# Optimization experiments

Measured on AMD Instinct MI355X. Metric: run time of the kernel, lower is better.

Reference implementation:

```python
import jax, jax.numpy as jnp
import numpy as np

V, E, H, L, B, T = 32000, 256, 512, 2, 64, 2048


def setup_inputs() -> dict:
    key = jax.random.key(0)
    ks = jax.random.split(key, 24)
    def rn(i, shape, scale=0.05):
        return jax.random.normal(ks[i], shape, jnp.float32) * scale
    inp = {
        "token": jax.random.randint(ks[0], (B,), 0, V),
        "h0": rn(1, (L, B, H), 1.0),
        "c0": rn(2, (L, B, H), 1.0),
        "encoder_outputs": rn(3, (B, T, H), 1.0),
        "mask": jax.random.randint(ks[4], (B, T), 0, 2).astype(jnp.int32),
        # parameters
        "emb_table": rn(5, (V, E), 1.0).at[0].set(0.0),  # padding_idx=0
        "W_attn": rn(6, (H, 2 * H)),
        "b_attn": rn(7, (H,)),
        "v_attn": jax.random.uniform(ks[8], (H,), jnp.float32),  # torch.rand init
        "W_ih0": rn(9, (4 * H, E + H)),
        "W_hh0": rn(10, (4 * H, H)),
        "b_ih0": rn(11, (4 * H,)),
        "b_hh0": rn(12, (4 * H,)),
        "W_ih1": rn(13, (4 * H, H)),
        "W_hh1": rn(14, (4 * H, H)),
        "b_ih1": rn(15, (4 * H,)),
        "b_hh1": rn(16, (4 * H,)),
        "W_out": rn(17, (V, H)),
        "b_out": rn(18, (V,)),
    }
    return inp


def _lstm_step(x, h, c, Wi, Wh, bi, bh):
    # PyTorch gate order: i, f, g, o
    gates = x @ Wi.T + bi + h @ Wh.T + bh  # [B, 4H]
    i, f, g, o = jnp.split(gates, 4, axis=-1)
    c_new = jax.nn.sigmoid(f) * c + jax.nn.sigmoid(i) * jnp.tanh(g)
    h_new = jax.nn.sigmoid(o) * jnp.tanh(c_new)
    return h_new, c_new


def reference(token, h0, c0, encoder_outputs, mask,
              emb_table, W_attn, b_attn, v_attn,
              W_ih0, W_hh0, b_ih0, b_hh0,
              W_ih1, W_hh1, b_ih1, b_hh1,
              W_out, b_out):
    embedded = emb_table[token]  # [B, E]

    # Bahdanau attention using the top-layer hidden state.
    # Linear on concat(hidden, enc) split into two matmuls (no T-tiling of hidden).
    h_top = h0[-1]  # [B, H]
    h_part = h_top @ W_attn[:, :H].T  # [B, H]
    e_part = jnp.einsum('bth,kh->btk', encoder_outputs, W_attn[:, H:])  # [B, T, H]
    energy = jnp.tanh(h_part[:, None, :] + e_part + b_attn) @ v_attn  # [B, T]
    energy = jnp.where(mask == 0, -jnp.inf, energy)
    attn_weights = jax.nn.softmax(energy, axis=1)  # [B, T]

    context = jnp.einsum('bt,bth->bh', attn_weights, encoder_outputs)  # [B, H]

    # Single-step 2-layer LSTM (eval mode: no inter-layer dropout).
    x0 = jnp.concatenate([embedded, context], axis=-1)  # [B, E+H]
    h0_new, c0_new = _lstm_step(x0, h0[0], c0[0], W_ih0, W_hh0, b_ih0, b_hh0)
    h1_new, c1_new = _lstm_step(h0_new, h0[1], c0[1], W_ih1, W_hh1, b_ih1, b_hh1)

    logits = h1_new @ W_out.T + b_out  # [B, V]
    h_new = jnp.stack([h0_new, h1_new])  # [L, B, H]
    c_new = jnp.stack([c0_new, c1_new])
    return logits, (h_new, c_new), attn_weights
```

## Files before the change

### kernel.cpp

```cpp
#include <hip/hip_runtime.h>
#include <hip/hip_fp16.h>
#include <cmath>

typedef _Float16 f16x8 __attribute__((ext_vector_type(8)));
typedef _Float16 f16x4 __attribute__((ext_vector_type(4)));
typedef float f32x4 __attribute__((ext_vector_type(4)));

#define NV 32000
#define NE 256
#define NH 512
#define NB 64
#define NT 2048

__device__ __forceinline__ float fast_tanh(float x) {
  return 1.f - 2.f / (__expf(2.f * x) + 1.f);
}
__device__ __forceinline__ float fast_sig(float x) {
  return 1.f / (1.f + __expf(-x));
}

__global__ void k_swz_be(const float* __restrict__ Wattn, _Float16* __restrict__ Be) {
  int idx = blockIdx.x * 256 + threadIdx.x;
  int l = idx & 63, nt = (idx >> 6) & 31, kc = idx >> 11;
  int n = (nt << 4) + (l & 15);
  int h0 = (kc << 5) + ((l >> 4) << 3);
  const float* s = Wattn + n * 1024 + 512 + h0;
  _Float16* d = Be + idx * 8;
  #pragma unroll
  for (int j = 0; j < 8; ++j) d[j] = (_Float16)s[j];
}

__global__ void k_prep_htop(const float* __restrict__ h0, _Float16* __restrict__ xh,
                            _Float16* __restrict__ xcat1) {
  int b = blockIdx.x, t = threadIdx.x;
  _Float16 v = (_Float16)h0[NB * NH + b * NH + t];
  xh[b * NH + t] = v;
  xcat1[b * 1024 + 512 + t] = v;
}

template <int KLEN>
__global__ __launch_bounds__(128)
void k_gemm_bT(const _Float16* __restrict__ A, int K,
               const float* __restrict__ B0, int ldb0,
               const float* __restrict__ B1, int ldb1, int b1k,
               const float* __restrict__ bias,
               float* __restrict__ out, int N) {
  int ntiles = N >> 5;
  int bn = blockIdx.x % ntiles, kcid = blockIdx.x / ntiles;
  int tid = threadIdx.x, w = tid >> 6, l = tid & 63;
  int n = (bn << 5) + (w << 4) + (l & 15);
  int kq = (l >> 4) << 3;
  int k0 = kcid * KLEN;
  f32x4 acc[4];
  #pragma unroll
  for (int mi = 0; mi < 4; ++mi) acc[mi] = (f32x4){0.f, 0.f, 0.f, 0.f};
  #pragma unroll 2
  for (int kk = 0; kk < KLEN; kk += 32) {
    int kbase = k0 + kk;
    f16x8 a[4];
    #pragma unroll
    for (int mi = 0; mi < 4; ++mi)
      a[mi] = *(const f16x8*)(A + (size_t)((l & 15) + (mi << 4)) * K + kbase + kq);
    const float* bp;
    if (B1 && kbase >= b1k) bp = B1 + (size_t)n * ldb1 + (kbase - b1k) + kq;
    else                    bp = B0 + (size_t)n * ldb0 + kbase + kq;
    float4 x0 = *(const float4*)bp;
    float4 x1 = *(const float4*)(bp + 4);
    f16x8 bf = {(_Float16)x0.x, (_Float16)x0.y, (_Float16)x0.z, (_Float16)x0.w,
                (_Float16)x1.x, (_Float16)x1.y, (_Float16)x1.z, (_Float16)x1.w};
    #pragma unroll
    for (int mi = 0; mi < 4; ++mi)
      acc[mi] = __builtin_amdgcn_mfma_f32_16x16x32_f16(a[mi], bf, acc[mi], 0, 0, 0);
  }
  float* op = out + (size_t)kcid * 64 * N;
  #pragma unroll
  for (int mi = 0; mi < 4; ++mi)
    #pragma unroll
    for (int r = 0; r < 4; ++r) {
      int row = (mi << 4) + ((l >> 4) << 2) + r;
      float v = acc[mi][r];
      if (bias) v += bias[n];
      op[(size_t)row * N + n] = v;
    }
}

__global__ __launch_bounds__(512, 4)
void k_energy(const float* __restrict__ enc, const _Float16* __restrict__ Be,
              const float* __restrict__ hp0, const float* __restrict__ hp1,
              const float* __restrict__ battn, const float* __restrict__ vat,
              const int* __restrict__ mask,
              float* __restrict__ eng, float* __restrict__ mcsc,
              float* __restrict__ numpart) {
  __shared__ _Float16 As[64 * 512];
  __shared__ float hpl[NH], vl[NH], ep[64][8], wl[64];
  int tile = blockIdx.x;
  int b = tile >> 5;
  long row0 = (long)tile << 6;
  int tid = threadIdx.x;
  hpl[tid] = hp0[(b << 9) + tid] + hp1[(b << 9) + tid] + battn[tid];
  vl[tid] = vat[tid];
  int w = tid >> 6, l = tid & 63;

  const float4* encp = (const float4*)(enc + row0 * NH);
  for (int half = 0; half < 2; ++half) {
    float4 st[8];
    #pragma unroll
    for (int i = 0; i < 8; ++i) st[i] = encp[tid + ((half * 8 + i) << 9)];
    #pragma unroll
    for (int i = 0; i < 8; ++i) {
      int s = tid + ((half * 8 + i) << 9);
      int r = s >> 7, c4 = s & 127;
      f16x4 h4 = {(_Float16)st[i].x, (_Float16)st[i].y,
                  (_Float16)st[i].z, (_Float16)st[i].w};
      *(f16x4*)((char*)As + (r << 10) + (((c4 << 3)) ^ ((r & 7) << 4))) = h4;
    }
  }
  __syncthreads();

  f32x4 acc[4][4];
  #pragma unroll
  for (int mi = 0; mi < 4; ++mi)
    #pragma unroll
    for (int ni = 0; ni < 4; ++ni) acc[mi][ni] = (f32x4){0.f, 0.f, 0.f, 0.f};

  for (int kc = 0; kc < 16; ++kc) {
    f16x8 a[4], bf[4];
    int kb = (kc << 6) + ((l >> 4) << 4);
    #pragma unroll
    for (int mi = 0; mi < 4; ++mi) {
      int r = (mi << 4) + (l & 15);
      a[mi] = *(const f16x8*)((char*)As + (r << 10) + (kb ^ ((r & 7) << 4)));
    }
    #pragma unroll
    for (int ni = 0; ni < 4; ++ni)
      bf[ni] = *(const f16x8*)(Be + (size_t)((((kc << 5) + (w << 2) + ni) << 6) + l) * 8);
    #pragma unroll
    for (int mi = 0; mi < 4; ++mi)
      #pragma unroll
      for (int ni = 0; ni < 4; ++ni)
        acc[mi][ni] = __builtin_amdgcn_mfma_f32_16x16x32_f16(a[mi], bf[ni], acc[mi][ni], 0, 0, 0);
  }

  int cl = l & 15;
  #pragma unroll
  for (int mi = 0; mi < 4; ++mi) {
    float s0 = 0.f, s1 = 0.f, s2 = 0.f, s3 = 0.f;
    #pragma unroll
    for (int ni = 0; ni < 4; ++ni) {
      int col = (w << 6) + (ni << 4) + cl;
      float hv = hpl[col], vv = vl[col];
      s0 += vv * fast_tanh(acc[mi][ni][0] + hv);
      s1 += vv * fast_tanh(acc[mi][ni][1] + hv);
      s2 += vv * fast_tanh(acc[mi][ni][2] + hv);
      s3 += vv * fast_tanh(acc[mi][ni][3] + hv);
    }
    #pragma unroll
    for (int off = 1; off < 16; off <<= 1) {
      s0 += __shfl_xor(s0, off, 64);
      s1 += __shfl_xor(s1, off, 64);
      s2 += __shfl_xor(s2, off, 64);
      s3 += __shfl_xor(s3, off, 64);
    }
    if (cl == 0) {
      int rb = (mi << 4) + ((l >> 4) << 2);
      ep[rb][w] = s0; ep[rb + 1][w] = s1; ep[rb + 2][w] = s2; ep[rb + 3][w] = s3;
    }
  }
  __syncthreads();

  if (tid < 64) {
    float e = 0.f;
    #pragma unroll
    for (int q = 0; q < 8; ++q) e += ep[tid][q];
    int mk = mask[row0 + tid];
    e = mk ? e : -3.0e38f;
    eng[row0 + tid] = e;
    float m = e;
    #pragma unroll
    for (int off = 32; off; off >>= 1) m = fmaxf(m, __shfl_xor(m, off, 64));
    float wv = mk ? __expf(e - m) : 0.f;
    float s = wv;
    #pragma unroll
    for (int off = 32; off; off >>= 1) s += __shfl_xor(s, off, 64);
    wl[tid] = wv;
    if (tid == 0) { mcsc[tile * 2] = m; mcsc[tile * 2 + 1] = s; }
  }
  __syncthreads();

  float a = 0.f;
  #pragma unroll 4
  for (int t = 0; t < 64; ++t) {
    float ev = (float)(*(const _Float16*)((char*)As + (t << 10) + (((tid * 2)) ^ ((t & 7) << 4))));
    a += wl[t] * ev;
  }
  numpart[(size_t)tile * NH + tid] = a;
}

__global__ void k_combine(const float* __restrict__ mcsc, const float* __restrict__ numpart,
                          const float* __restrict__ eng, const int* __restrict__ token,
                          const float* __restrict__ emb, const float* __restrict__ h0,
                          _Float16* __restrict__ xcat0, float* __restrict__ attw) {
  __shared__ float scale_s[32], Ms, dens;
  int b = blockIdx.x, tid = threadIdx.x;
  if (tid < 32) {
    float m = mcsc[(b * 32 + tid) * 2];
    float s = mcsc[(b * 32 + tid) * 2 + 1];
    float M = m;
    #pragma unroll
    for (int off = 16; off; off >>= 1) M = fmaxf(M, __shfl_xor(M, off, 32));
    float sc = __expf(m - M);
    float d = sc * s;
    #pragma unroll
    for (int off = 16; off; off >>= 1) d += __shfl_xor(d, off, 32);
    scale_s[tid] = sc;
    if (tid == 0) { Ms = M; dens = d; }
  }
  __syncthreads();
  float M = Ms, rden = 1.f / dens;
  float a = 0.f;
  #pragma unroll 4
  for (int c = 0; c < 32; ++c) a += scale_s[c] * numpart[(size_t)(b * 32 + c) * NH + tid];
  xcat0[b * 1280 + 256 + tid] = (_Float16)(a * rden);
  if (tid < 256) xcat0[b * 1280 + tid] = (_Float16)emb[(size_t)token[b] * NE + tid];
  xcat0[b * 1280 + 768 + tid] = (_Float16)h0[b * NH + tid];
  #pragma unroll
  for (int i = 0; i < 4; ++i) {
    int t = tid + (i << 9);
    attw[(b << 11) + t] = __expf(eng[(b << 11) + t] - M) * rden;
  }
}

__global__ void k_act(const float* __restrict__ pg, const float* __restrict__ bih,
                      const float* __restrict__ bhh, const float* __restrict__ cprev,
                      float* __restrict__ hout, float* __restrict__ cout,
                      _Float16* __restrict__ hf16, int hpitch, int nchunks) {
  int idx = blockIdx.x * 256 + threadIdx.x;
  int b = idx >> 9, u = idx & 511;
  float g[4];
  #pragma unroll
  for (int gi = 0; gi < 4; ++gi) {
    float s = bih[gi * 512 + u] + bhh[gi * 512 + u];
    for (int kc = 0; kc < nchunks; ++kc)
      s += pg[((size_t)kc * 64 + b) * 2048 + gi * 512 + u];
    g[gi] = s;
  }
  float c = fast_sig(g[1]) * cprev[idx] + fast_sig(g[0]) * fast_tanh(g[2]);
  float h = fast_sig(g[3]) * fast_tanh(c);
  cout[idx] = c;
  hout[idx] = h;
  hf16[b * hpitch + u] = (_Float16)h;
}

extern "C" void kernel_launch(void* const* d_in, const int* in_sizes, int n_in,
                              void* d_out, int out_size, void* d_ws, size_t ws_size,
                              hipStream_t stream) {
  (void)in_sizes; (void)n_in; (void)out_size; (void)ws_size;
  const int*   token = (const int*)d_in[0];
  const float* h0    = (const float*)d_in[1];
  const float* c0    = (const float*)d_in[2];
  const float* enc   = (const float*)d_in[3];
  const int*   mask  = (const int*)d_in[4];
  const float* emb   = (const float*)d_in[5];
  const float* Wattn = (const float*)d_in[6];
  const float* battn = (const float*)d_in[7];
  const float* vattn = (const float*)d_in[8];
  const float* Wih0  = (const float*)d_in[9];
  const float* Whh0  = (const float*)d_in[10];
  const float* bih0  = (const float*)d_in[11];
  const float* bhh0  = (const float*)d_in[12];
  const float* Wih1  = (const float*)d_in[13];
  const float* Whh1  = (const float*)d_in[14];
  const float* bih1  = (const float*)d_in[15];
  const float* bhh1  = (const float*)d_in[16];
  const float* Wout  = (const float*)d_in[17];
  const float* bout  = (const float*)d_in[18];

  float* ws    = (float*)d_ws;
  float* pghp  = ws;
  float* eng   = pghp + 65536;
  float* mcsc  = eng + 131072;
  float* np    = mcsc + 4096;
  float* pg0   = np + 1048576;
  float* pg1   = pg0 + 524288;
  _Float16* Be    = (_Float16*)(pg1 + 524288);
  _Float16* xh    = Be + 262144;
  _Float16* xcat0 = xh + 32768;
  _Float16* xcat1 = xcat0 + 81920;
  _Float16* h1f   = xcat1 + 65536;

  float* out    = (float*)d_out;
  float* logits = out;
  float* hnew   = out + (size_t)NB * NV;
  float* cnew   = hnew + 2 * NB * NH;
  float* attw   = cnew + 2 * NB * NH;

  k_swz_be<<<dim3(128), dim3(256), 0, stream>>>(Wattn, Be);
  k_prep_htop<<<dim3(64), dim3(512), 0, stream>>>(h0, xh, xcat1);
  k_gemm_bT<256><<<dim3(32), dim3(128), 0, stream>>>(
      xh, NH, Wattn, 1024, nullptr, 0, 1 << 30, nullptr, pghp, NH);
  k_energy<<<dim3(2048), dim3(512), 0, stream>>>(
      enc, Be, pghp, pghp + 32768, battn, vattn, mask, eng, mcsc, np);
  k_combine<<<dim3(64), dim3(512), 0, stream>>>(
      mcsc, np, eng, token, emb, h0, xcat0, attw);
  k_gemm_bT<320><<<dim3(256), dim3(128), 0, stream>>>(
      xcat0, 1280, Wih0, 768, Whh0, NH, 768, nullptr, pg0, 2048);
  k_act<<<dim3(128), dim3(256), 0, stream>>>(
      pg0, bih0, bhh0, c0, hnew, cnew, xcat1, 1024, 4);
  k_gemm_bT<256><<<dim3(256), dim3(128), 0, stream>>>(
      xcat1, 1024, Wih1, NH, Whh1, NH, NH, nullptr, pg1, 2048);
  k_act<<<dim3(128), dim3(256), 0, stream>>>(
      pg1, bih1, bhh1, c0 + NB * NH, hnew + NB * NH, cnew + NB * NH, h1f, 512, 4);
  k_gemm_bT<512><<<dim3(1000), dim3(128), 0, stream>>>(
      h1f, NH, Wout, NH, nullptr, 0, 1 << 30, bout, logits, NV);
}
```

Baseline: 193.6 us.

## Stream encoder tile from global into MFMA fragments instead of LDS staging

The energy kernel no longer converts the whole 64x512 encoder tile to fp16 in shared memory. Each wave now loads its A fragments straight from global memory and converts them in registers, using a 2x4 wave grid with 2x8 MFMA tiles per wave. The context partial sum is recomputed in fp32 by re-reading the encoder rows from global memory, which is expected to hit cache, and is reduced through a small shared buffer. This frees about 64KB of LDS per block to raise occupancy and removes the staging barrier. The cost is strided global fragment loads and a second pass over the encoder tile.

```diff
diff --git a/kernel.cpp b/kernel.cpp
--- a/kernel.cpp
+++ b/kernel.cpp
@@ -91,63 +91,52 @@
               const int* __restrict__ mask,
               float* __restrict__ eng, float* __restrict__ mcsc,
               float* __restrict__ numpart) {
-  __shared__ _Float16 As[64 * 512];
-  __shared__ float hpl[NH], vl[NH], ep[64][8], wl[64];
+  __shared__ float hpl[NH], vl[NH], ep[64][4], wl[64], psc[4][NH];
   int tile = blockIdx.x;
   int b = tile >> 5;
   long row0 = (long)tile << 6;
-  int tid = threadIdx.x;
+  int tid = threadIdx.x, w = tid >> 6, l = tid & 63;
+  int wm = w >> 2, wn = w & 3;
   hpl[tid] = hp0[(b << 9) + tid] + hp1[(b << 9) + tid] + battn[tid];
   vl[tid] = vat[tid];
-  int w = tid >> 6, l = tid & 63;
-
-  const float4* encp = (const float4*)(enc + row0 * NH);
-  for (int half = 0; half < 2; ++half) {
-    float4 st[8];
-    #pragma unroll
-    for (int i = 0; i < 8; ++i) st[i] = encp[tid + ((half * 8 + i) << 9)];
-    #pragma unroll
-    for (int i = 0; i < 8; ++i) {
-      int s = tid + ((half * 8 + i) << 9);
-      int r = s >> 7, c4 = s & 127;
-      f16x4 h4 = {(_Float16)st[i].x, (_Float16)st[i].y,
-                  (_Float16)st[i].z, (_Float16)st[i].w};
-      *(f16x4*)((char*)As + (r << 10) + (((c4 << 3)) ^ ((r & 7) << 4))) = h4;
-    }
-  }
   __syncthreads();
 
-  f32x4 acc[4][4];
-  #pragma unroll
-  for (int mi = 0; mi < 4; ++mi)
-    #pragma unroll
-    for (int ni = 0; ni < 4; ++ni) acc[mi][ni] = (f32x4){0.f, 0.f, 0.f, 0.f};
-
+  const float* Ab = enc + (row0 + (wm << 5) + (l & 15)) * NH + ((l >> 4) << 3);
+  f32x4 acc[2][8];
+  #pragma unroll
+  for (int mi = 0; mi < 2; ++mi)
+    #pragma unroll
+    for (int ni = 0; ni < 8; ++ni) acc[mi][ni] = (f32x4){0.f, 0.f, 0.f, 0.f};
+
+  #pragma unroll 2
   for (int kc = 0; kc < 16; ++kc) {
-    f16x8 a[4], bf[4];
-    int kb = (kc << 6) + ((l >> 4) << 4);
-    #pragma unroll
-    for (int mi = 0; mi < 4; ++mi) {
-      int r = (mi << 4) + (l & 15);
-      a[mi] = *(const f16x8*)((char*)As + (r << 10) + (kb ^ ((r & 7) << 4)));
-    }
-    #pragma unroll
-    for (int ni = 0; ni < 4; ++ni)
-      bf[ni] = *(const f16x8*)(Be + (size_t)((((kc << 5) + (w << 2) + ni) << 6) + l) * 8);
-    #pragma unroll
-    for (int mi = 0; mi < 4; ++mi)
-      #pragma unroll
-      for (int ni = 0; ni < 4; ++ni)
-        acc[mi][ni] = __builtin_amdgcn_mfma_f32_16x16x32_f16(a[mi], bf[ni], acc[mi][ni], 0, 0, 0);
+    f16x8 afr[2];
+    #pragma unroll
+    for (int mi = 0; mi < 2; ++mi) {
+      const float* ap = Ab + (size_t)(mi << 4) * NH + (kc << 5);
+      f32x4 lo = *(const f32x4*)ap;
+      f32x4 hi = *(const f32x4*)(ap + 4);
+      afr[mi] = (f16x8){(_Float16)lo[0], (_Float16)lo[1],
+                        (_Float16)lo[2], (_Float16)lo[3],
+                        (_Float16)hi[0], (_Float16)hi[1],
+                        (_Float16)hi[2], (_Float16)hi[3]};
+    }
+    #pragma unroll
+    for (int ni = 0; ni < 8; ++ni) {
+      f16x8 bfr = *(const f16x8*)(Be +
+          (size_t)((((kc << 5) + (wn << 3) + ni) << 6) + l) * 8);
+      acc[0][ni] = __builtin_amdgcn_mfma_f32_16x16x32_f16(afr[0], bfr, acc[0][ni], 0, 0, 0);
+      acc[1][ni] = __builtin_amdgcn_mfma_f32_16x16x32_f16(afr[1], bfr, acc[1][ni], 0, 0, 0);
+    }
   }
 
   int cl = l & 15;
   #pragma unroll
-  for (int mi = 0; mi < 4; ++mi) {
+  for (int mi = 0; mi < 2; ++mi) {
     float s0 = 0.f, s1 = 0.f, s2 = 0.f, s3 = 0.f;
     #pragma unroll
-    for (int ni = 0; ni < 4; ++ni) {
-      int col = (w << 6) + (ni << 4) + cl;
+    for (int ni = 0; ni < 8; ++ni) {
+      int col = (wn << 7) + (ni << 4) + cl;
       float hv = hpl[col], vv = vl[col];
       s0 += vv * fast_tanh(acc[mi][ni][0] + hv);
       s1 += vv * fast_tanh(acc[mi][ni][1] + hv);
@@ -162,19 +151,18 @@
       s3 += __shfl_xor(s3, off, 64);
     }
     if (cl == 0) {
-      int rb = (mi << 4) + ((l >> 4) << 2);
-      ep[rb][w] = s0; ep[rb + 1][w] = s1; ep[rb + 2][w] = s2; ep[rb + 3][w] = s3;
+      int rb = (wm << 5) + (mi << 4) + ((l >> 4) << 2);
+      ep[rb][wn] = s0; ep[rb + 1][wn] = s1; ep[rb + 2][wn] = s2; ep[rb + 3][wn] = s3;
     }
   }
   __syncthreads();
 
-  if (tid < 64) {
-    float e = 0.f;
-    #pragma unroll
-    for (int q = 0; q < 8; ++q) e += ep[tid][q];
-    int mk = mask[row0 + tid];
+  {
+    float4 e4 = *(const float4*)&ep[l][0];
+    float e = (e4.x + e4.y) + (e4.z + e4.w);
+    int mk = mask[row0 + l];
     e = mk ? e : -3.0e38f;
-    eng[row0 + tid] = e;
+    if (w == 0) eng[row0 + l] = e;
     float m = e;
     #pragma unroll
     for (int off = 32; off; off >>= 1) m = fmaxf(m, __shfl_xor(m, off, 64));
@@ -182,18 +170,26 @@
     float s = wv;
     #pragma unroll
     for (int off = 32; off; off >>= 1) s += __shfl_xor(s, off, 64);
-    wl[tid] = wv;
+    wl[l] = wv;
     if (tid == 0) { mcsc[tile * 2] = m; mcsc[tile * 2 + 1] = s; }
   }
+
+  {
+    int rg = tid >> 7, j4 = tid & 127;
+    const float* gp = enc + (row0 + (rg << 4)) * NH + (j4 << 2);
+    float c0a = 0.f, c1a = 0.f, c2a = 0.f, c3a = 0.f;
+    #pragma unroll 4
+    for (int r16 = 0; r16 < 16; ++r16) {
+      float4 ev = *(const float4*)(gp + (size_t)r16 * NH);
+      float wv = wl[(rg << 4) + r16];
+      c0a += wv * ev.x; c1a += wv * ev.y; c2a += wv * ev.z; c3a += wv * ev.w;
+    }
+    *(float4*)&psc[rg][j4 << 2] = (float4){c0a, c1a, c2a, c3a};
+  }
   __syncthreads();
 
-  float a = 0.f;
-  #pragma unroll 4
-  for (int t = 0; t < 64; ++t) {
-    float ev = (float)(*(const _Float16*)((char*)As + (t << 10) + (((tid * 2)) ^ ((t & 7) << 4))));
-    a += wl[t] * ev;
-  }
-  numpart[(size_t)tile * NH + tid] = a;
+  numpart[(size_t)tile * NH + tid] =
+      psc[0][tid] + psc[1][tid] + psc[2][tid] + psc[3][tid];
 }
 
 __global__ void k_combine(const float* __restrict__ mcsc, const float* __restrict__ numpart,
```

Measured after the change: 304.2 us. 57.1% more time.
